# Kernel optimization log

Hardware: AMD Instinct MI355X
Metric: run time of the kernel (lower is better)

## Reference

```python
import jax, jax.numpy as jnp
import numpy as np

ALPHA = 0.2  # LeakyReLU negative slope


def setup_inputs() -> dict:
    key = jax.random.key(0)
    k1, k2, k3, k4 = jax.random.split(key, 4)
    N, Fin, Fout = 8192, 256, 64
    inputs = {
        "input": jax.random.normal(k1, (N, Fin), dtype=jnp.float32),
        "adj": jax.random.randint(k2, (N, N), 0, 2, dtype=jnp.int32),
        "W": jax.random.normal(k3, (Fin, Fout), dtype=jnp.float32) * (1.414 * np.sqrt(2.0 / (Fin + Fout))),
        "a": jax.random.normal(k4, (2 * Fout, 1), dtype=jnp.float32) * (1.414 * np.sqrt(2.0 / (2 * Fout + 1))),
    }
    return inputs


def reference(input, adj, W, a):
    # h: [N, Fout]
    h = input @ W
    Fout = h.shape[1]
    # Decompose pairwise score: e[i,j] = leakyrelu(h[i]@a1 + h[j]@a2)
    # (mathematically identical to the original concat+matmul construction,
    #  but avoids the O(N^2 * 2F) intermediate)
    a1, a2 = a[:Fout, 0], a[Fout:, 0]
    s1 = h @ a1  # [N]
    s2 = h @ a2  # [N]
    e = jax.nn.leaky_relu(s1[:, None] + s2[None, :], negative_slope=ALPHA)  # [N, N]
    # Mask non-edges with -10 (as in the original), row softmax
    masked = jnp.where(adj > 0, e, jnp.float32(-10.0))
    attention = jax.nn.softmax(masked, axis=1)
    # dropout p=0.0 (eval/reference mode): identity
    h_prime = attention @ h  # [N, Fout]
    return jax.nn.elu(h_prime)  # concat=True path
```

## Files before the change

kernel.cpp:

```cpp
#include <hip/hip_runtime.h>
#include <hip/hip_bf16.h>
#include <cstdint>
#include <cstddef>

#define NN 8192
#define FIN 256
#define FOUT 64
#define ALPHA_SLOPE 0.2f
#define EXP_M10 4.5399929762484854e-05f

#define JSPLIT 8
#define CP 68

typedef short s16x8 __attribute__((ext_vector_type(8)));
typedef float f32x4 __attribute__((ext_vector_type(4)));

__device__ __forceinline__ unsigned short f2bf(float x) {
    union { float f; uint32_t u; } v; v.f = x;
    uint32_t u = v.u;
    return (unsigned short)((u + 0x7FFFu + ((u >> 16) & 1u)) >> 16);
}

__global__ __launch_bounds__(256) void k_h(
    const float* __restrict__ input, const float* __restrict__ W,
    const float* __restrict__ a,
    unsigned short* __restrict__ htg, float* __restrict__ s1, float* __restrict__ s2)
{
    __shared__ __align__(16) unsigned short tile[64][28];
    const int wid  = threadIdx.x >> 6;
    const int lane = threadIdx.x & 63;
    const int i0   = blockIdx.x * 16;
    const int r0   = wid * 4;
    const float* inb = input + (size_t)(i0 + r0) * FIN;

    float acc0 = 0.f, acc1 = 0.f, acc2 = 0.f, acc3 = 0.f;
    #pragma unroll 4
    for (int c = 0; c < FIN; c += 4) {
        float w0 = W[(c + 0) * FOUT + lane];
        float w1 = W[(c + 1) * FOUT + lane];
        float w2 = W[(c + 2) * FOUT + lane];
        float w3 = W[(c + 3) * FOUT + lane];
        float4 x0 = *(const float4*)(inb + 0 * FIN + c);
        float4 x1 = *(const float4*)(inb + 1 * FIN + c);
        float4 x2 = *(const float4*)(inb + 2 * FIN + c);
        float4 x3 = *(const float4*)(inb + 3 * FIN + c);
        acc0 = fmaf(x0.x, w0, fmaf(x0.y, w1, fmaf(x0.z, w2, fmaf(x0.w, w3, acc0))));
        acc1 = fmaf(x1.x, w0, fmaf(x1.y, w1, fmaf(x1.z, w2, fmaf(x1.w, w3, acc1))));
        acc2 = fmaf(x2.x, w0, fmaf(x2.y, w1, fmaf(x2.z, w2, fmaf(x2.w, w3, acc2))));
        acc3 = fmaf(x3.x, w0, fmaf(x3.y, w1, fmaf(x3.z, w2, fmaf(x3.w, w3, acc3))));
    }

    const float a1v = a[lane], a2v = a[FOUT + lane];
    float accs[4] = {acc0, acc1, acc2, acc3};
    #pragma unroll
    for (int r = 0; r < 4; ++r) {
        float v1 = accs[r] * a1v;
        float v2 = accs[r] * a2v;
        #pragma unroll
        for (int off = 32; off; off >>= 1) {
            v1 += __shfl_xor(v1, off);
            v2 += __shfl_xor(v2, off);
        }
        if (lane == 0) { s1[i0 + r0 + r] = v1; s2[i0 + r0 + r] = v2; }
        tile[lane][r0 + r] = f2bf(accs[r]);
    }
    __syncthreads();

    const int feat = threadIdx.x >> 2;
    const int cg   = (threadIdx.x & 3) * 4;
    uint2 q = *(const uint2*)&tile[feat][cg];
    *(uint2*)(htg + (size_t)feat * NN + i0 + cg) = q;
}

__global__ __launch_bounds__(256) void k_attn(
    const int* __restrict__ adj,
    const unsigned short* __restrict__ htg,
    const float* __restrict__ s1g, const float* __restrict__ s2g,
    float* __restrict__ slabs)
{
    const int t    = threadIdx.x;
    const int wid  = t >> 6;
    const int lane = t & 63;
    const int gw   = blockIdx.x * 4 + wid;
    const int mi   = gw >> 3;
    const int js   = gw & 7;
    const int m    = lane & 15;
    const int quad = lane >> 4;
    const int irow = mi * 16 + m;
    const int jb   = js * (NN / JSPLIT) + quad * 8;

    const float s1v = s1g[irow];

    const short bd = (m == 0) ? (short)0x3F80 : (short)0;
    const s16x8 bden = {bd, bd, bd, bd, bd, bd, bd, bd};

    f32x4 acc0 = {0,0,0,0}, acc1 = {0,0,0,0}, acc2 = {0,0,0,0},
          acc3 = {0,0,0,0}, acc4 = {0,0,0,0};

    const int*   aptr = adj + (size_t)irow * NN + jb;
    const float* s2p  = s2g + jb;
    const unsigned short* h0 = htg + (size_t)(m +  0) * NN + jb;
    const unsigned short* h1 = htg + (size_t)(m + 16) * NN + jb;
    const unsigned short* h2 = htg + (size_t)(m + 32) * NN + jb;
    const unsigned short* h3 = htg + (size_t)(m + 48) * NN + jb;

    #pragma unroll 2
    for (int ko = 0; ko < (NN / JSPLIT) / 32; ++ko) {
        int4   av0 = *(const int4*)(aptr);
        int4   av1 = *(const int4*)(aptr + 4);
        float4 sa  = *(const float4*)(s2p);
        float4 sb  = *(const float4*)(s2p + 4);
        s16x8  b0  = *(const s16x8*)(h0);
        s16x8  b1  = *(const s16x8*)(h1);
        s16x8  b2  = *(const s16x8*)(h2);
        s16x8  b3  = *(const s16x8*)(h3);

        float x0 = s1v + sa.x, x1 = s1v + sa.y, x2 = s1v + sa.z, x3 = s1v + sa.w;
        float x4 = s1v + sb.x, x5 = s1v + sb.y, x6 = s1v + sb.z, x7 = s1v + sb.w;
        float w0 = (av0.x > 0) ? __expf(fmaxf(x0, ALPHA_SLOPE * x0)) : EXP_M10;
        float w1 = (av0.y > 0) ? __expf(fmaxf(x1, ALPHA_SLOPE * x1)) : EXP_M10;
        float w2 = (av0.z > 0) ? __expf(fmaxf(x2, ALPHA_SLOPE * x2)) : EXP_M10;
        float w3 = (av0.w > 0) ? __expf(fmaxf(x3, ALPHA_SLOPE * x3)) : EXP_M10;
        float w4 = (av1.x > 0) ? __expf(fmaxf(x4, ALPHA_SLOPE * x4)) : EXP_M10;
        float w5 = (av1.y > 0) ? __expf(fmaxf(x5, ALPHA_SLOPE * x5)) : EXP_M10;
        float w6 = (av1.z > 0) ? __expf(fmaxf(x6, ALPHA_SLOPE * x6)) : EXP_M10;
        float w7 = (av1.w > 0) ? __expf(fmaxf(x7, ALPHA_SLOPE * x7)) : EXP_M10;

        s16x8 af;
        af[0] = (short)f2bf(w0); af[1] = (short)f2bf(w1);
        af[2] = (short)f2bf(w2); af[3] = (short)f2bf(w3);
        af[4] = (short)f2bf(w4); af[5] = (short)f2bf(w5);
        af[6] = (short)f2bf(w6); af[7] = (short)f2bf(w7);

        acc0 = __builtin_amdgcn_mfma_f32_16x16x32_bf16(af, b0,   acc0, 0, 0, 0);
        acc1 = __builtin_amdgcn_mfma_f32_16x16x32_bf16(af, b1,   acc1, 0, 0, 0);
        acc2 = __builtin_amdgcn_mfma_f32_16x16x32_bf16(af, b2,   acc2, 0, 0, 0);
        acc3 = __builtin_amdgcn_mfma_f32_16x16x32_bf16(af, b3,   acc3, 0, 0, 0);
        acc4 = __builtin_amdgcn_mfma_f32_16x16x32_bf16(af, bden, acc4, 0, 0, 0);

        aptr += 32; s2p += 32; h0 += 32; h1 += 32; h2 += 32; h3 += 32;
    }

    float* slab = slabs + (size_t)js * ((size_t)NN * CP);
    const int r0 = mi * 16 + quad * 4;
    #pragma unroll
    for (int reg = 0; reg < 4; ++reg) {
        size_t ro = (size_t)(r0 + reg) * CP;
        slab[ro +  0 + m] = acc0[reg];
        slab[ro + 16 + m] = acc1[reg];
        slab[ro + 32 + m] = acc2[reg];
        slab[ro + 48 + m] = acc3[reg];
        if (m == 0) slab[ro + 64] = acc4[reg];
    }
}

__global__ __launch_bounds__(256) void k_norm(
    const float* __restrict__ slabs, float* __restrict__ out)
{
    int gid = blockIdx.x * 256 + threadIdx.x;
    int i = gid >> 6, k = gid & 63;
    float num = 0.f, den = 0.f;
    #pragma unroll
    for (int js = 0; js < JSPLIT; ++js) {
        const float* row = slabs + (size_t)js * ((size_t)NN * CP) + (size_t)i * CP;
        num += row[k];
        den += row[64];
    }
    float v = num / den;
    out[gid] = (v > 0.f) ? v : (__expf(v) - 1.f);
}

extern "C" void kernel_launch(void* const* d_in, const int* in_sizes, int n_in,
                              void* d_out, int out_size, void* d_ws, size_t ws_size,
                              hipStream_t stream) {
    const float* input = (const float*)d_in[0];
    const int*   adj   = (const int*)d_in[1];
    const float* W     = (const float*)d_in[2];
    const float* a     = (const float*)d_in[3];
    float* out = (float*)d_out;

    char* ws = (char*)d_ws;
    float* slabs = (float*)ws;
    size_t off = (size_t)JSPLIT * NN * CP * sizeof(float);
    unsigned short* htg = (unsigned short*)(ws + off);
    off += (size_t)FOUT * NN * sizeof(unsigned short);
    float* s1 = (float*)(ws + off); off += NN * sizeof(float);
    float* s2 = (float*)(ws + off);

    k_h   <<<NN / 16, 256, 0, stream>>>(input, W, a, htg, s1, s2);
    k_attn<<<(NN / 16) * JSPLIT / 4, 256, 0, stream>>>(adj, htg, s1, s2, slabs);
    k_norm<<<NN * FOUT / 256, 256, 0, stream>>>(slabs, out);
}
```

Baseline: 455.1 us.

## Stage attention weights and h tiles in LDS with double-buffered strips

Restructures the attention kernel so each 512-thread block handles 128 rows and one j-split. The block cooperatively computes the bf16 softmax weights and loads h-transposed tiles into padded LDS, with double buffering across 64-column strips. The h tile is shared by all eight waves instead of each wave re-reading it from global memory. The cost is a block-wide barrier per strip, larger LDS use, and fewer, bigger blocks.

```diff
diff --git a/kernel.cpp b/kernel.cpp
--- a/kernel.cpp
+++ b/kernel.cpp
@@ -10,15 +10,35 @@
 #define EXP_M10 4.5399929762484854e-05f
 
 #define JSPLIT 8
+#define STRIP 64
+#define NSTRIP ((NN / JSPLIT) / STRIP)
+#define RB 128
+#define WPITCH 144
+#define HPITCH 144
 #define CP 68
 
 typedef short s16x8 __attribute__((ext_vector_type(8)));
 typedef float f32x4 __attribute__((ext_vector_type(4)));
+typedef int   i32x4 __attribute__((ext_vector_type(4)));
 
 __device__ __forceinline__ unsigned short f2bf(float x) {
     union { float f; uint32_t u; } v; v.f = x;
     uint32_t u = v.u;
     return (unsigned short)((u + 0x7FFFu + ((u >> 16) & 1u)) >> 16);
+}
+
+__device__ __forceinline__ unsigned int pk2(float lo, float hi) {
+    return (unsigned int)f2bf(lo) | ((unsigned int)f2bf(hi) << 16);
+}
+
+__device__ __forceinline__ uint2 wpack4(i32x4 a, float4 v, float s1v) {
+    float x0 = s1v + v.x, x1 = s1v + v.y, x2 = s1v + v.z, x3 = s1v + v.w;
+    float w0 = (a.x > 0) ? __expf(fmaxf(x0, ALPHA_SLOPE * x0)) : EXP_M10;
+    float w1 = (a.y > 0) ? __expf(fmaxf(x1, ALPHA_SLOPE * x1)) : EXP_M10;
+    float w2 = (a.z > 0) ? __expf(fmaxf(x2, ALPHA_SLOPE * x2)) : EXP_M10;
+    float w3 = (a.w > 0) ? __expf(fmaxf(x3, ALPHA_SLOPE * x3)) : EXP_M10;
+    uint2 r; r.x = pk2(w0, w1); r.y = pk2(w2, w3);
+    return r;
 }
 
 __global__ __launch_bounds__(256) void k_h(
@@ -72,77 +92,110 @@
     *(uint2*)(htg + (size_t)feat * NN + i0 + cg) = q;
 }
 
-__global__ __launch_bounds__(256) void k_attn(
+__global__ __launch_bounds__(512, 4) void k_attn(
     const int* __restrict__ adj,
     const unsigned short* __restrict__ htg,
     const float* __restrict__ s1g, const float* __restrict__ s2g,
     float* __restrict__ slabs)
 {
+    __shared__ __align__(16) unsigned char wbuf[2][RB * WPITCH];
+    __shared__ __align__(16) unsigned char hbuf[2][64 * HPITCH];
+
     const int t    = threadIdx.x;
     const int wid  = t >> 6;
     const int lane = t & 63;
-    const int gw   = blockIdx.x * 4 + wid;
-    const int mi   = gw >> 3;
-    const int js   = gw & 7;
+    const int bi   = blockIdx.x >> 3;
+    const int js   = blockIdx.x & 7;
+    const int i0   = bi * RB;
+    const int jbase = js * (NN / JSPLIT);
     const int m    = lane & 15;
     const int quad = lane >> 4;
-    const int irow = mi * 16 + m;
-    const int jb   = js * (NN / JSPLIT) + quad * 8;
-
-    const float s1v = s1g[irow];
+
+    const int srow  = t >> 2;
+    const int scol  = (t & 3) * 16;
+    const int sfeat = t >> 3;
+    const int scol2 = (t & 7) * 8;
+    const float s1v = s1g[i0 + srow];
 
     const short bd = (m == 0) ? (short)0x3F80 : (short)0;
     const s16x8 bden = {bd, bd, bd, bd, bd, bd, bd, bd};
 
     f32x4 acc0 = {0,0,0,0}, acc1 = {0,0,0,0}, acc2 = {0,0,0,0},
-          acc3 = {0,0,0,0}, acc4 = {0,0,0,0};
-
-    const int*   aptr = adj + (size_t)irow * NN + jb;
-    const float* s2p  = s2g + jb;
-    const unsigned short* h0 = htg + (size_t)(m +  0) * NN + jb;
-    const unsigned short* h1 = htg + (size_t)(m + 16) * NN + jb;
-    const unsigned short* h2 = htg + (size_t)(m + 32) * NN + jb;
-    const unsigned short* h3 = htg + (size_t)(m + 48) * NN + jb;
-
-    #pragma unroll 2
-    for (int ko = 0; ko < (NN / JSPLIT) / 32; ++ko) {
-        int4   av0 = *(const int4*)(aptr);
-        int4   av1 = *(const int4*)(aptr + 4);
-        float4 sa  = *(const float4*)(s2p);
-        float4 sb  = *(const float4*)(s2p + 4);
-        s16x8  b0  = *(const s16x8*)(h0);
-        s16x8  b1  = *(const s16x8*)(h1);
-        s16x8  b2  = *(const s16x8*)(h2);
-        s16x8  b3  = *(const s16x8*)(h3);
-
-        float x0 = s1v + sa.x, x1 = s1v + sa.y, x2 = s1v + sa.z, x3 = s1v + sa.w;
-        float x4 = s1v + sb.x, x5 = s1v + sb.y, x6 = s1v + sb.z, x7 = s1v + sb.w;
-        float w0 = (av0.x > 0) ? __expf(fmaxf(x0, ALPHA_SLOPE * x0)) : EXP_M10;
-        float w1 = (av0.y > 0) ? __expf(fmaxf(x1, ALPHA_SLOPE * x1)) : EXP_M10;
-        float w2 = (av0.z > 0) ? __expf(fmaxf(x2, ALPHA_SLOPE * x2)) : EXP_M10;
-        float w3 = (av0.w > 0) ? __expf(fmaxf(x3, ALPHA_SLOPE * x3)) : EXP_M10;
-        float w4 = (av1.x > 0) ? __expf(fmaxf(x4, ALPHA_SLOPE * x4)) : EXP_M10;
-        float w5 = (av1.y > 0) ? __expf(fmaxf(x5, ALPHA_SLOPE * x5)) : EXP_M10;
-        float w6 = (av1.z > 0) ? __expf(fmaxf(x6, ALPHA_SLOPE * x6)) : EXP_M10;
-        float w7 = (av1.w > 0) ? __expf(fmaxf(x7, ALPHA_SLOPE * x7)) : EXP_M10;
-
-        s16x8 af;
-        af[0] = (short)f2bf(w0); af[1] = (short)f2bf(w1);
-        af[2] = (short)f2bf(w2); af[3] = (short)f2bf(w3);
-        af[4] = (short)f2bf(w4); af[5] = (short)f2bf(w5);
-        af[6] = (short)f2bf(w6); af[7] = (short)f2bf(w7);
-
-        acc0 = __builtin_amdgcn_mfma_f32_16x16x32_bf16(af, b0,   acc0, 0, 0, 0);
-        acc1 = __builtin_amdgcn_mfma_f32_16x16x32_bf16(af, b1,   acc1, 0, 0, 0);
-        acc2 = __builtin_amdgcn_mfma_f32_16x16x32_bf16(af, b2,   acc2, 0, 0, 0);
-        acc3 = __builtin_amdgcn_mfma_f32_16x16x32_bf16(af, b3,   acc3, 0, 0, 0);
-        acc4 = __builtin_amdgcn_mfma_f32_16x16x32_bf16(af, bden, acc4, 0, 0, 0);
-
-        aptr += 32; s2p += 32; h0 += 32; h1 += 32; h2 += 32; h3 += 32;
+          acc3 = {0,0,0,0}, accD = {0,0,0,0};
+
+    const int* adjrow = adj + (size_t)(i0 + srow) * NN + jbase;
+    const unsigned short* hrow = htg + (size_t)sfeat * NN + jbase;
+
+    {
+        i32x4  a0 = *(const i32x4*)(adjrow + scol);
+        i32x4  a1 = *(const i32x4*)(adjrow + scol + 4);
+        i32x4  a2 = *(const i32x4*)(adjrow + scol + 8);
+        i32x4  a3 = *(const i32x4*)(adjrow + scol + 12);
+        float4 v0 = *(const float4*)(s2g + jbase + scol);
+        float4 v1 = *(const float4*)(s2g + jbase + scol + 4);
+        float4 v2 = *(const float4*)(s2g + jbase + scol + 8);
+        float4 v3 = *(const float4*)(s2g + jbase + scol + 12);
+        s16x8  h0 = *(const s16x8*)(hrow + scol2);
+
+        uint2 pA = wpack4(a0, v0, s1v), pB = wpack4(a1, v1, s1v);
+        uint2 pC = wpack4(a2, v2, s1v), pD = wpack4(a3, v3, s1v);
+        uint4 q0 = {pA.x, pA.y, pB.x, pB.y};
+        uint4 q1 = {pC.x, pC.y, pD.x, pD.y};
+        unsigned char* wd = &wbuf[0][srow * WPITCH + (t & 3) * 32];
+        *(uint4*)(wd)      = q0;
+        *(uint4*)(wd + 16) = q1;
+        *(s16x8*)&hbuf[0][sfeat * HPITCH + scol2 * 2] = h0;
+    }
+    __syncthreads();
+
+    for (int s = 0; s < NSTRIP; ++s) {
+        const int cur = s & 1, nxt = cur ^ 1;
+        const bool more = (s + 1 < NSTRIP);
+
+        i32x4 a0, a1, a2, a3; float4 v0, v1, v2, v3; s16x8 h0;
+        if (more) {
+            const int jn = (s + 1) * STRIP;
+            a0 = *(const i32x4*)(adjrow + jn + scol);
+            a1 = *(const i32x4*)(adjrow + jn + scol + 4);
+            a2 = *(const i32x4*)(adjrow + jn + scol + 8);
+            a3 = *(const i32x4*)(adjrow + jn + scol + 12);
+            v0 = *(const float4*)(s2g + jbase + jn + scol);
+            v1 = *(const float4*)(s2g + jbase + jn + scol + 4);
+            v2 = *(const float4*)(s2g + jbase + jn + scol + 8);
+            v3 = *(const float4*)(s2g + jbase + jn + scol + 12);
+            h0 = *(const s16x8*)(hrow + jn + scol2);
+        }
+
+        #pragma unroll
+        for (int kk = 0; kk < 2; ++kk) {
+            const int cb = kk * 64 + quad * 16;
+            s16x8 af = *(const s16x8*)&wbuf[cur][(wid * 16 + m) * WPITCH + cb];
+            s16x8 b0 = *(const s16x8*)&hbuf[cur][(m +  0) * HPITCH + cb];
+            s16x8 b1 = *(const s16x8*)&hbuf[cur][(m + 16) * HPITCH + cb];
+            s16x8 b2 = *(const s16x8*)&hbuf[cur][(m + 32) * HPITCH + cb];
+            s16x8 b3 = *(const s16x8*)&hbuf[cur][(m + 48) * HPITCH + cb];
+            acc0 = __builtin_amdgcn_mfma_f32_16x16x32_bf16(af, b0,   acc0, 0, 0, 0);
+            acc1 = __builtin_amdgcn_mfma_f32_16x16x32_bf16(af, b1,   acc1, 0, 0, 0);
+            acc2 = __builtin_amdgcn_mfma_f32_16x16x32_bf16(af, b2,   acc2, 0, 0, 0);
+            acc3 = __builtin_amdgcn_mfma_f32_16x16x32_bf16(af, b3,   acc3, 0, 0, 0);
+            accD = __builtin_amdgcn_mfma_f32_16x16x32_bf16(af, bden, accD, 0, 0, 0);
+        }
+
+        if (more) {
+            uint2 pA = wpack4(a0, v0, s1v), pB = wpack4(a1, v1, s1v);
+            uint2 pC = wpack4(a2, v2, s1v), pD = wpack4(a3, v3, s1v);
+            uint4 q0 = {pA.x, pA.y, pB.x, pB.y};
+            uint4 q1 = {pC.x, pC.y, pD.x, pD.y};
+            unsigned char* wd = &wbuf[nxt][srow * WPITCH + (t & 3) * 32];
+            *(uint4*)(wd)      = q0;
+            *(uint4*)(wd + 16) = q1;
+            *(s16x8*)&hbuf[nxt][sfeat * HPITCH + scol2 * 2] = h0;
+        }
+        __syncthreads();
     }
 
     float* slab = slabs + (size_t)js * ((size_t)NN * CP);
-    const int r0 = mi * 16 + quad * 4;
+    const int r0 = i0 + wid * 16 + quad * 4;
     #pragma unroll
     for (int reg = 0; reg < 4; ++reg) {
         size_t ro = (size_t)(r0 + reg) * CP;
@@ -150,7 +203,7 @@
         slab[ro + 16 + m] = acc1[reg];
         slab[ro + 32 + m] = acc2[reg];
         slab[ro + 48 + m] = acc3[reg];
-        if (m == 0) slab[ro + 64] = acc4[reg];
+        if (m == 0) slab[ro + 64] = accD[reg];
     }
 }
 
@@ -188,6 +241,6 @@
     float* s2 = (float*)(ws + off);
 
     k_h   <<<NN / 16, 256, 0, stream>>>(input, W, a, htg, s1, s2);
-    k_attn<<<(NN / 16) * JSPLIT / 4, 256, 0, stream>>>(adj, htg, s1, s2, slabs);
+    k_attn<<<(NN / RB) * JSPLIT, 512, 0, stream>>>(adj, htg, s1, s2, slabs);
     k_norm<<<NN * FOUT / 256, 256, 0, stream>>>(slabs, out);
 }
```

Measured after the change: 421.9 us. 1.08x faster.

## Stage h^T and s2 tiles in LDS, compute softmax denominator with scalar sums

Applied to the files above, without the earlier changes.

k_attn now runs 512-thread blocks that each cover 128 rows and one j-slice. Each block first stages that slice's bf16 h^T tile (padded pitch) and its s2 values in shared memory, so all 8 waves reuse them instead of each reloading them from global memory. The fifth MFMA that computed the denominator is replaced by an fp32 sum of the rounded bf16 weights, reduced across quads with shuffles. This trades a large LDS allocation (~132KB), which lowers occupancy, plus a startup sync, for less global traffic and fewer MFMAs. The adj stream, likely the dominant cost, is unchanged.

```diff
diff --git a/kernel.cpp b/kernel.cpp
--- a/kernel.cpp
+++ b/kernel.cpp
@@ -10,15 +10,34 @@
 #define EXP_M10 4.5399929762484854e-05f
 
 #define JSPLIT 8
+#define JRANGE (NN / JSPLIT)
+#define KITER (JRANGE / 32)
+#define RB 128
+#define HT_PITCH 2064
 #define CP 68
 
 typedef short s16x8 __attribute__((ext_vector_type(8)));
 typedef float f32x4 __attribute__((ext_vector_type(4)));
+typedef int   i32x4 __attribute__((ext_vector_type(4)));
 
 __device__ __forceinline__ unsigned short f2bf(float x) {
     union { float f; uint32_t u; } v; v.f = x;
     uint32_t u = v.u;
     return (unsigned short)((u + 0x7FFFu + ((u >> 16) & 1u)) >> 16);
+}
+
+__device__ __forceinline__ unsigned int rpack2(float a, float b, float& dsum) {
+    union { float f; uint32_t u; } va, vb, ra, rb;
+    va.f = a; vb.f = b;
+    ra.u = (va.u + 0x7FFFu + ((va.u >> 16) & 1u)) & 0xFFFF0000u;
+    rb.u = (vb.u + 0x7FFFu + ((vb.u >> 16) & 1u)) & 0xFFFF0000u;
+    dsum += ra.f + rb.f;
+    return (ra.u >> 16) | rb.u;
+}
+
+__device__ __forceinline__ float wval(int a, float s2v, float s1v) {
+    float x = s1v + s2v;
+    return (a > 0) ? __expf(fmaxf(x, ALPHA_SLOPE * x)) : EXP_M10;
 }
 
 __global__ __launch_bounds__(256) void k_h(
@@ -72,77 +91,70 @@
     *(uint2*)(htg + (size_t)feat * NN + i0 + cg) = q;
 }
 
-__global__ __launch_bounds__(256) void k_attn(
+__global__ __launch_bounds__(512) void k_attn(
     const int* __restrict__ adj,
     const unsigned short* __restrict__ htg,
     const float* __restrict__ s1g, const float* __restrict__ s2g,
     float* __restrict__ slabs)
 {
+    __shared__ __align__(16) unsigned char hlds[64 * HT_PITCH];
+    __shared__ __align__(16) float s2buf[JRANGE];
+
     const int t    = threadIdx.x;
     const int wid  = t >> 6;
     const int lane = t & 63;
-    const int gw   = blockIdx.x * 4 + wid;
-    const int mi   = gw >> 3;
-    const int js   = gw & 7;
+    const int bi   = blockIdx.x >> 3;
+    const int js   = blockIdx.x & 7;
+    const int i0   = bi * RB;
+    const int jbase = js * JRANGE;
     const int m    = lane & 15;
     const int quad = lane >> 4;
-    const int irow = mi * 16 + m;
-    const int jb   = js * (NN / JSPLIT) + quad * 8;
-
+
+    #pragma unroll
+    for (int c = t; c < 64 * (JRANGE / 8); c += 512) {
+        const int row = c >> 7;
+        const int col = c & 127;
+        *(s16x8*)&hlds[row * HT_PITCH + col * 16] =
+            *(const s16x8*)(htg + (size_t)row * NN + jbase + col * 8);
+    }
+    if (t < JRANGE / 4)
+        *(float4*)&s2buf[t * 4] = *(const float4*)(s2g + jbase + t * 4);
+    __syncthreads();
+
+    const int irow = i0 + wid * 16 + m;
     const float s1v = s1g[irow];
-
-    const short bd = (m == 0) ? (short)0x3F80 : (short)0;
-    const s16x8 bden = {bd, bd, bd, bd, bd, bd, bd, bd};
-
-    f32x4 acc0 = {0,0,0,0}, acc1 = {0,0,0,0}, acc2 = {0,0,0,0},
-          acc3 = {0,0,0,0}, acc4 = {0,0,0,0};
-
-    const int*   aptr = adj + (size_t)irow * NN + jb;
-    const float* s2p  = s2g + jb;
-    const unsigned short* h0 = htg + (size_t)(m +  0) * NN + jb;
-    const unsigned short* h1 = htg + (size_t)(m + 16) * NN + jb;
-    const unsigned short* h2 = htg + (size_t)(m + 32) * NN + jb;
-    const unsigned short* h3 = htg + (size_t)(m + 48) * NN + jb;
-
-    #pragma unroll 2
-    for (int ko = 0; ko < (NN / JSPLIT) / 32; ++ko) {
-        int4   av0 = *(const int4*)(aptr);
-        int4   av1 = *(const int4*)(aptr + 4);
-        float4 sa  = *(const float4*)(s2p);
-        float4 sb  = *(const float4*)(s2p + 4);
-        s16x8  b0  = *(const s16x8*)(h0);
-        s16x8  b1  = *(const s16x8*)(h1);
-        s16x8  b2  = *(const s16x8*)(h2);
-        s16x8  b3  = *(const s16x8*)(h3);
-
-        float x0 = s1v + sa.x, x1 = s1v + sa.y, x2 = s1v + sa.z, x3 = s1v + sa.w;
-        float x4 = s1v + sb.x, x5 = s1v + sb.y, x6 = s1v + sb.z, x7 = s1v + sb.w;
-        float w0 = (av0.x > 0) ? __expf(fmaxf(x0, ALPHA_SLOPE * x0)) : EXP_M10;
-        float w1 = (av0.y > 0) ? __expf(fmaxf(x1, ALPHA_SLOPE * x1)) : EXP_M10;
-        float w2 = (av0.z > 0) ? __expf(fmaxf(x2, ALPHA_SLOPE * x2)) : EXP_M10;
-        float w3 = (av0.w > 0) ? __expf(fmaxf(x3, ALPHA_SLOPE * x3)) : EXP_M10;
-        float w4 = (av1.x > 0) ? __expf(fmaxf(x4, ALPHA_SLOPE * x4)) : EXP_M10;
-        float w5 = (av1.y > 0) ? __expf(fmaxf(x5, ALPHA_SLOPE * x5)) : EXP_M10;
-        float w6 = (av1.z > 0) ? __expf(fmaxf(x6, ALPHA_SLOPE * x6)) : EXP_M10;
-        float w7 = (av1.w > 0) ? __expf(fmaxf(x7, ALPHA_SLOPE * x7)) : EXP_M10;
-
-        s16x8 af;
-        af[0] = (short)f2bf(w0); af[1] = (short)f2bf(w1);
-        af[2] = (short)f2bf(w2); af[3] = (short)f2bf(w3);
-        af[4] = (short)f2bf(w4); af[5] = (short)f2bf(w5);
-        af[6] = (short)f2bf(w6); af[7] = (short)f2bf(w7);
-
-        acc0 = __builtin_amdgcn_mfma_f32_16x16x32_bf16(af, b0,   acc0, 0, 0, 0);
-        acc1 = __builtin_amdgcn_mfma_f32_16x16x32_bf16(af, b1,   acc1, 0, 0, 0);
-        acc2 = __builtin_amdgcn_mfma_f32_16x16x32_bf16(af, b2,   acc2, 0, 0, 0);
-        acc3 = __builtin_amdgcn_mfma_f32_16x16x32_bf16(af, b3,   acc3, 0, 0, 0);
-        acc4 = __builtin_amdgcn_mfma_f32_16x16x32_bf16(af, bden, acc4, 0, 0, 0);
-
-        aptr += 32; s2p += 32; h0 += 32; h1 += 32; h2 += 32; h3 += 32;
+    const int* ap = adj + (size_t)irow * NN + jbase + quad * 8;
+
+    f32x4 acc0 = {0,0,0,0}, acc1 = {0,0,0,0}, acc2 = {0,0,0,0}, acc3 = {0,0,0,0};
+    float dsum = 0.f;
+
+    #pragma unroll 4
+    for (int kk = 0; kk < KITER; ++kk) {
+        i32x4 a0 = *(const i32x4*)(ap + kk * 32);
+        i32x4 a1 = *(const i32x4*)(ap + kk * 32 + 4);
+
+        const int cb = (kk * 32 + quad * 8) * 2;
+        s16x8 b0 = *(const s16x8*)&hlds[(m +  0) * HT_PITCH + cb];
+        s16x8 b1 = *(const s16x8*)&hlds[(m + 16) * HT_PITCH + cb];
+        s16x8 b2 = *(const s16x8*)&hlds[(m + 32) * HT_PITCH + cb];
+        s16x8 b3 = *(const s16x8*)&hlds[(m + 48) * HT_PITCH + cb];
+        float4 v0 = *(const float4*)&s2buf[kk * 32 + quad * 8];
+        float4 v1 = *(const float4*)&s2buf[kk * 32 + quad * 8 + 4];
+
+        union { uint4 u; s16x8 v; } af;
+        af.u.x = rpack2(wval(a0.x, v0.x, s1v), wval(a0.y, v0.y, s1v), dsum);
+        af.u.y = rpack2(wval(a0.z, v0.z, s1v), wval(a0.w, v0.w, s1v), dsum);
+        af.u.z = rpack2(wval(a1.x, v1.x, s1v), wval(a1.y, v1.y, s1v), dsum);
+        af.u.w = rpack2(wval(a1.z, v1.z, s1v), wval(a1.w, v1.w, s1v), dsum);
+
+        acc0 = __builtin_amdgcn_mfma_f32_16x16x32_bf16(af.v, b0, acc0, 0, 0, 0);
+        acc1 = __builtin_amdgcn_mfma_f32_16x16x32_bf16(af.v, b1, acc1, 0, 0, 0);
+        acc2 = __builtin_amdgcn_mfma_f32_16x16x32_bf16(af.v, b2, acc2, 0, 0, 0);
+        acc3 = __builtin_amdgcn_mfma_f32_16x16x32_bf16(af.v, b3, acc3, 0, 0, 0);
     }
 
     float* slab = slabs + (size_t)js * ((size_t)NN * CP);
-    const int r0 = mi * 16 + quad * 4;
+    const int r0 = i0 + wid * 16 + quad * 4;
     #pragma unroll
     for (int reg = 0; reg < 4; ++reg) {
         size_t ro = (size_t)(r0 + reg) * CP;
@@ -150,8 +162,10 @@
         slab[ro + 16 + m] = acc1[reg];
         slab[ro + 32 + m] = acc2[reg];
         slab[ro + 48 + m] = acc3[reg];
-        if (m == 0) slab[ro + 64] = acc4[reg];
-    }
+    }
+    dsum += __shfl_xor(dsum, 16);
+    dsum += __shfl_xor(dsum, 32);
+    if (quad == 0) slab[(size_t)irow * CP + 64] = dsum;
 }
 
 __global__ __launch_bounds__(256) void k_norm(
@@ -188,6 +202,6 @@
     float* s2 = (float*)(ws + off);
 
     k_h   <<<NN / 16, 256, 0, stream>>>(input, W, a, htg, s1, s2);
-    k_attn<<<(NN / 16) * JSPLIT / 4, 256, 0, stream>>>(adj, htg, s1, s2, slabs);
+    k_attn<<<(NN / RB) * JSPLIT, 512, 0, stream>>>(adj, htg, s1, s2, slabs);
     k_norm<<<NN * FOUT / 256, 256, 0, stream>>>(slabs, out);
 }
```

Result: faster. 428.2 us (-5.9%).
